# Kernel tuning notes

Hardware: AMD Instinct MI355X
Metric: run time of the kernel (lower is better)

The kernel has to match this reference:

```python
import jax, jax.numpy as jnp
import numpy as np

BN_EPS = 1e-5
SAMPLE_KEY = jax.random.key(42)


def setup_inputs() -> dict:
    key = jax.random.key(0)
    ks = jax.random.split(key, 12)
    B, W, E = 524288, 8, 4
    D = W * E  # 32, input dim of fc1

    def lin(k, fan_in, fan_out):
        k1, k2 = jax.random.split(k)
        bound = 1.0 / np.sqrt(fan_in)
        w = jax.random.uniform(k1, (fan_in, fan_out), jnp.float32, -bound, bound)
        b = jax.random.uniform(k2, (fan_out,), jnp.float32, -bound, bound)
        return w, b

    W1, b1 = lin(ks[0], D, 50)
    W2, b2 = lin(ks[1], 50, 30)
    W3, b3 = lin(ks[2], 30, 20)
    W4, b4 = lin(ks[3], 20, 15)
    W5, b5 = lin(ks[4], 15, W)
    # BatchNorm affine params (eval mode, running_mean=0, running_var=1)
    g1, be1 = jnp.ones((50,), jnp.float32), jnp.zeros((50,), jnp.float32)
    g2, be2 = jnp.ones((30,), jnp.float32), jnp.zeros((30,), jnp.float32)
    g3, be3 = jnp.ones((20,), jnp.float32), jnp.zeros((20,), jnp.float32)
    events = jax.random.normal(ks[5], (B, W, E), jnp.float32)
    return {"events": events,
            "W1": W1, "b1": b1, "g1": g1, "be1": be1,
            "W2": W2, "b2": b2, "g2": g2, "be2": be2,
            "W3": W3, "b3": b3, "g3": g3, "be3": be3,
            "W4": W4, "b4": b4, "W5": W5, "b5": b5}


def _bn_eval(x, g, b):
    # eval-mode BatchNorm1d with running_mean=0, running_var=1
    return x * (g / jnp.sqrt(1.0 + BN_EPS)) + b


def _probs(events, W1, b1, g1, be1, W2, b2, g2, be2, W3, b3, g3, be3, W4, b4, W5, b5):
    B = events.shape[0]
    x = events.reshape(B, -1)  # (B, window*event_size)
    h = jax.nn.relu(_bn_eval(x @ W1 + b1, g1, be1))
    h = jax.nn.relu(_bn_eval(h @ W2 + b2, g2, be2))
    h = jax.nn.relu(_bn_eval(h @ W3 + b3, g3, be3))
    h = jax.nn.relu(h @ W4 + b4)
    return jax.nn.sigmoid(h @ W5 + b5)  # (B, window_size)


def reference(events, W1, b1, g1, be1, W2, b2, g2, be2, W3, b3, g3, be3, W4, b4, W5, b5):
    p = _probs(events, W1, b1, g1, be1, W2, b2, g2, be2, W3, b3, g3, be3, W4, b4, W5, b5)
    # np.random.choice([0,1], p=[p, 1-p]) => P(choice=1) = 1 - p
    choice = jax.random.bernoulli(SAMPLE_KEY, 1.0 - p).astype(p.dtype)  # (B, W)
    chosen_events_np = 1.0 - choice
    flipped = jnp.abs(choice - p)            # prob of sampled outcome per element
    log_prob = jnp.log(jnp.prod(flipped, axis=1))  # (B,)
    return chosen_events_np, log_prob
```

## Files before the change

### kernel.cpp

```cpp
#include <hip/hip_runtime.h>
#include <math.h>

#define THREADS 256
#define P_MARGIN 1e-4f
#define FIXCAP 32

typedef float v2f __attribute__((ext_vector_type(2)));

__device__ __forceinline__ void tf2x32(unsigned x0, unsigned x1,
                                       unsigned &o0, unsigned &o1) {
  const unsigned k0 = 0u;
  const unsigned k1 = 42u;
  const unsigned k2 = 0x1BD11BDAu ^ k0 ^ k1;
  x0 += k0; x1 += k1;
#define TF_R(r) { x0 += x1; x1 = (x1 << (r)) | (x1 >> (32 - (r))); x1 ^= x0; }
  TF_R(13) TF_R(15) TF_R(26) TF_R(6)
  x0 += k1; x1 += k2 + 1u;
  TF_R(17) TF_R(29) TF_R(16) TF_R(24)
  x0 += k2; x1 += k0 + 2u;
  TF_R(13) TF_R(15) TF_R(26) TF_R(6)
  x0 += k0; x1 += k1 + 3u;
  TF_R(17) TF_R(29) TF_R(16) TF_R(24)
  x0 += k1; x1 += k2 + 4u;
  TF_R(13) TF_R(15) TF_R(26) TF_R(6)
  x0 += k2; x1 += k0 + 5u;
#undef TF_R
  o0 = x0; o1 = x1;
}

__global__ __launch_bounds__(THREADS, 4)
void wtf_kernel(const float* __restrict__ events,
                const float* __restrict__ W1, const float* __restrict__ b1,
                const float* __restrict__ g1, const float* __restrict__ be1,
                const float* __restrict__ W2, const float* __restrict__ b2,
                const float* __restrict__ g2, const float* __restrict__ be2,
                const float* __restrict__ W3, const float* __restrict__ b3,
                const float* __restrict__ g3, const float* __restrict__ be3,
                const float* __restrict__ W4, const float* __restrict__ b4,
                const float* __restrict__ W5, const float* __restrict__ b5,
                float* __restrict__ out_chosen,
                float* __restrict__ out_logp,
                int B) {
  __shared__ unsigned s_cnt;
  __shared__ unsigned s_rows[FIXCAP];
  __shared__ double sA[64];
  __shared__ double sB[64];
  __shared__ double sF[8];

  const int t = threadIdx.x;
  if (t == 0) s_cnt = 0;
  __syncthreads();

  const int b = blockIdx.x * THREADS + t;
  const bool active = (b < B);
  const float rden = (float)(1.0 / sqrt(1.0 + 1e-5));

  if (active) {
    float x[32];
    const float4* ev4 = reinterpret_cast<const float4*>(events) + (size_t)b * 8;
#pragma unroll
    for (int q = 0; q < 8; ++q) {
      float4 v = ev4[q];
      x[4 * q + 0] = v.x; x[4 * q + 1] = v.y; x[4 * q + 2] = v.z; x[4 * q + 3] = v.w;
    }

    v2f A[25];
#pragma unroll
    for (int j = 0; j < 25; ++j) A[j] = v2f{b1[2 * j], b1[2 * j + 1]};
#pragma unroll
    for (int k = 0; k < 32; ++k) {
      const v2f xk2 = {x[k], x[k]};
#pragma unroll
      for (int j = 0; j < 25; ++j) {
        v2f w = {W1[k * 50 + 2 * j], W1[k * 50 + 2 * j + 1]};
        A[j] = __builtin_elementwise_fma(xk2, w, A[j]);
      }
    }
    float a1[50];
#pragma unroll
    for (int j = 0; j < 25; ++j) {
      a1[2 * j + 0] = fmaxf(fmaf(A[j].x, g1[2 * j + 0] * rden, be1[2 * j + 0]), 0.f);
      a1[2 * j + 1] = fmaxf(fmaf(A[j].y, g1[2 * j + 1] * rden, be1[2 * j + 1]), 0.f);
    }

    v2f C[15];
#pragma unroll
    for (int j = 0; j < 15; ++j) C[j] = v2f{b2[2 * j], b2[2 * j + 1]};
#pragma unroll
    for (int k = 0; k < 50; ++k) {
      const v2f hk2 = {a1[k], a1[k]};
#pragma unroll
      for (int j = 0; j < 15; ++j) {
        v2f w = {W2[k * 30 + 2 * j], W2[k * 30 + 2 * j + 1]};
        C[j] = __builtin_elementwise_fma(hk2, w, C[j]);
      }
    }
    float a2[30];
#pragma unroll
    for (int j = 0; j < 15; ++j) {
      a2[2 * j + 0] = fmaxf(fmaf(C[j].x, g2[2 * j + 0] * rden, be2[2 * j + 0]), 0.f);
      a2[2 * j + 1] = fmaxf(fmaf(C[j].y, g2[2 * j + 1] * rden, be2[2 * j + 1]), 0.f);
    }

    v2f D[10];
#pragma unroll
    for (int j = 0; j < 10; ++j) D[j] = v2f{b3[2 * j], b3[2 * j + 1]};
#pragma unroll
    for (int k = 0; k < 30; ++k) {
      const v2f hk2 = {a2[k], a2[k]};
#pragma unroll
      for (int j = 0; j < 10; ++j) {
        v2f w = {W3[k * 20 + 2 * j], W3[k * 20 + 2 * j + 1]};
        D[j] = __builtin_elementwise_fma(hk2, w, D[j]);
      }
    }
    float a3[20];
#pragma unroll
    for (int j = 0; j < 10; ++j) {
      a3[2 * j + 0] = fmaxf(fmaf(D[j].x, g3[2 * j + 0] * rden, be3[2 * j + 0]), 0.f);
      a3[2 * j + 1] = fmaxf(fmaf(D[j].y, g3[2 * j + 1] * rden, be3[2 * j + 1]), 0.f);
    }

    v2f E[7];
    float e14 = b4[14];
#pragma unroll
    for (int j = 0; j < 7; ++j) E[j] = v2f{b4[2 * j], b4[2 * j + 1]};
#pragma unroll
    for (int k = 0; k < 20; ++k) {
      const float hk = a3[k];
      const v2f hk2 = {hk, hk};
#pragma unroll
      for (int j = 0; j < 7; ++j) {
        v2f w = {W4[k * 15 + 2 * j], W4[k * 15 + 2 * j + 1]};
        E[j] = __builtin_elementwise_fma(hk2, w, E[j]);
      }
      e14 = fmaf(hk, W4[k * 15 + 14], e14);
    }
    float a4[15];
#pragma unroll
    for (int j = 0; j < 7; ++j) {
      a4[2 * j + 0] = fmaxf(E[j].x, 0.f);
      a4[2 * j + 1] = fmaxf(E[j].y, 0.f);
    }
    a4[14] = fmaxf(e14, 0.f);

    v2f P[4];
#pragma unroll
    for (int j = 0; j < 4; ++j) P[j] = v2f{b5[2 * j], b5[2 * j + 1]};
#pragma unroll
    for (int k = 0; k < 15; ++k) {
      const v2f hk2 = {a4[k], a4[k]};
#pragma unroll
      for (int j = 0; j < 4; ++j) {
        v2f w = {W5[k * 8 + 2 * j], W5[k * 8 + 2 * j + 1]};
        P[j] = __builtin_elementwise_fma(hk2, w, P[j]);
      }
    }
    float p[8];
#pragma unroll
    for (int j = 0; j < 4; ++j) {
      p[2 * j + 0] = 1.f / (1.f + expf(-P[j].x));
      p[2 * j + 1] = 1.f / (1.f + expf(-P[j].y));
    }

    bool need = false;
    float prod = 1.f;
    float ch[8];
#pragma unroll
    for (int w = 0; w < 8; ++w) {
      unsigned j = 8u * (unsigned)b + (unsigned)w, o0, o1;
      tf2x32(0u, j, o0, o1);
      unsigned bits = o0 ^ o1;
      float u = __uint_as_float(0x3F800000u | (bits >> 9)) - 1.f;
      float thr = 1.f - p[w];
      bool choice = u < thr;
      need = need || (fabsf(u - thr) < P_MARGIN);
      ch[w] = choice ? 0.f : 1.f;
      prod *= choice ? thr : p[w];
    }
    if (need) {
      unsigned i = atomicAdd(&s_cnt, 1u);
      if (i < FIXCAP) s_rows[i] = (unsigned)b;
    }

    float4* oc = reinterpret_cast<float4*>(out_chosen) + (size_t)b * 2;
    oc[0] = make_float4(ch[0], ch[1], ch[2], ch[3]);
    oc[1] = make_float4(ch[4], ch[5], ch[6], ch[7]);
    out_logp[b] = logf(prod);
  }

  __syncthreads();
  unsigned cnt = s_cnt;
  if (cnt > FIXCAP) cnt = FIXCAP;
  if (cnt == 0) return;

  const double denom = sqrt(1.0 + 1e-5);
  for (unsigned r = 0; r < cnt; ++r) {
    const int rb = (int)s_rows[r];

    if (t < 32) sA[t] = (double)events[(size_t)rb * 32 + t];
    __syncthreads();

    double v = 0.0;
    if (t < 50) {
#pragma unroll
      for (int k = 0; k < 32; ++k) v = fma(sA[k], (double)W1[k * 50 + t], v);
      v += (double)b1[t];
      v = v * ((double)g1[t] / denom) + (double)be1[t];
      v = v > 0.0 ? v : 0.0;
    }
    __syncthreads();
    if (t < 50) sB[t] = v;
    __syncthreads();

    v = 0.0;
    if (t < 30) {
#pragma unroll
      for (int k = 0; k < 50; ++k) v = fma(sB[k], (double)W2[k * 30 + t], v);
      v += (double)b2[t];
      v = v * ((double)g2[t] / denom) + (double)be2[t];
      v = v > 0.0 ? v : 0.0;
    }
    __syncthreads();
    if (t < 30) sA[t] = v;
    __syncthreads();

    v = 0.0;
    if (t < 20) {
#pragma unroll
      for (int k = 0; k < 30; ++k) v = fma(sA[k], (double)W3[k * 20 + t], v);
      v += (double)b3[t];
      v = v * ((double)g3[t] / denom) + (double)be3[t];
      v = v > 0.0 ? v : 0.0;
    }
    __syncthreads();
    if (t < 20) sB[t] = v;
    __syncthreads();

    v = 0.0;
    if (t < 15) {
#pragma unroll
      for (int k = 0; k < 20; ++k) v = fma(sB[k], (double)W4[k * 15 + t], v);
      v += (double)b4[t];
      v = v > 0.0 ? v : 0.0;
    }
    __syncthreads();
    if (t < 15) sA[t] = v;
    __syncthreads();

    if (t < 8) {
      v = 0.0;
#pragma unroll
      for (int k = 0; k < 15; ++k) v = fma(sA[k], (double)W5[k * 8 + t], v);
      v += (double)b5[t];
      double p = 1.0 / (1.0 + exp(-v));
      unsigned j = 8u * (unsigned)rb + (unsigned)t, o0, o1;
      tf2x32(0u, j, o0, o1);
      unsigned bits = o0 ^ o1;
      float u = __uint_as_float(0x3F800000u | (bits >> 9)) - 1.f;
      double thr = 1.0 - p;
      bool choice = ((double)u < thr);
      out_chosen[(size_t)rb * 8 + t] = choice ? 0.f : 1.f;
      sF[t] = choice ? thr : p;
    }
    __syncthreads();
    if (t == 0) {
      double prod = 1.0;
      for (int w = 0; w < 8; ++w) prod *= sF[w];
      out_logp[rb] = (float)log(prod);
    }
    __syncthreads();
  }
}

extern "C" void kernel_launch(void* const* d_in, const int* in_sizes, int n_in,
                              void* d_out, int out_size, void* d_ws, size_t ws_size,
                              hipStream_t stream) {
  const float* events = (const float*)d_in[0];
  const float* W1  = (const float*)d_in[1];
  const float* b1  = (const float*)d_in[2];
  const float* g1  = (const float*)d_in[3];
  const float* be1 = (const float*)d_in[4];
  const float* W2  = (const float*)d_in[5];
  const float* b2  = (const float*)d_in[6];
  const float* g2  = (const float*)d_in[7];
  const float* be2 = (const float*)d_in[8];
  const float* W3  = (const float*)d_in[9];
  const float* b3  = (const float*)d_in[10];
  const float* g3  = (const float*)d_in[11];
  const float* be3 = (const float*)d_in[12];
  const float* W4  = (const float*)d_in[13];
  const float* b4  = (const float*)d_in[14];
  const float* W5  = (const float*)d_in[15];
  const float* b5  = (const float*)d_in[16];

  const int B = in_sizes[0] / 32;
  float* out = (float*)d_out;
  float* out_chosen = out;
  float* out_logp   = out + (size_t)B * 8;

  const int blocks = (B + THREADS - 1) / THREADS;
  hipLaunchKernelGGL(wtf_kernel, dim3(blocks), dim3(THREADS), 0, stream,
                     events, W1, b1, g1, be1, W2, b2, g2, be2,
                     W3, b3, g3, be3, W4, b4, W5, b5,
                     out_chosen, out_logp, B);
}
```

Baseline: 234.2 us.

## Split borderline-sample fixup into a separate kernel using a global worklist

The fused kernel is split in two. The fast kernel computes the fp32 MLP and sampling, then appends borderline rows to a global worklist in workspace through a global atomic. A second small kernel recomputes only those rows in double precision, spread across 512 blocks. This removes the shared-memory bookkeeping and block-wide barriers from the hot kernel and stops one block from serializing its own fixups, at the cost of an extra memset and kernel launch.

Measured after the change: 236.5 us. No clear change (+1.0%).

```diff
diff --git a/kernel.cpp b/kernel.cpp
--- a/kernel.cpp
+++ b/kernel.cpp
@@ -3,7 +3,6 @@
 
 #define THREADS 256
 #define P_MARGIN 1e-4f
-#define FIXCAP 32
 
 typedef float v2f __attribute__((ext_vector_type(2)));
 
@@ -29,176 +28,188 @@
 }
 
 __global__ __launch_bounds__(THREADS, 4)
-void wtf_kernel(const float* __restrict__ events,
-                const float* __restrict__ W1, const float* __restrict__ b1,
-                const float* __restrict__ g1, const float* __restrict__ be1,
-                const float* __restrict__ W2, const float* __restrict__ b2,
-                const float* __restrict__ g2, const float* __restrict__ be2,
-                const float* __restrict__ W3, const float* __restrict__ b3,
-                const float* __restrict__ g3, const float* __restrict__ be3,
-                const float* __restrict__ W4, const float* __restrict__ b4,
-                const float* __restrict__ W5, const float* __restrict__ b5,
-                float* __restrict__ out_chosen,
-                float* __restrict__ out_logp,
-                int B) {
-  __shared__ unsigned s_cnt;
-  __shared__ unsigned s_rows[FIXCAP];
+void wtf_fast_kernel(const float* __restrict__ events,
+                     const float* __restrict__ W1, const float* __restrict__ b1,
+                     const float* __restrict__ g1, const float* __restrict__ be1,
+                     const float* __restrict__ W2, const float* __restrict__ b2,
+                     const float* __restrict__ g2, const float* __restrict__ be2,
+                     const float* __restrict__ W3, const float* __restrict__ b3,
+                     const float* __restrict__ g3, const float* __restrict__ be3,
+                     const float* __restrict__ W4, const float* __restrict__ b4,
+                     const float* __restrict__ W5, const float* __restrict__ b5,
+                     float* __restrict__ out_chosen,
+                     float* __restrict__ out_logp,
+                     unsigned* __restrict__ fixlist,
+                     unsigned fixcap,
+                     int B) {
+  const int b = blockIdx.x * THREADS + threadIdx.x;
+  if (b >= B) return;
+
+  const float rden = (float)(1.0 / sqrt(1.0 + 1e-5));
+
+  float x[32];
+  const float4* ev4 = reinterpret_cast<const float4*>(events) + (size_t)b * 8;
+#pragma unroll
+  for (int q = 0; q < 8; ++q) {
+    float4 v = ev4[q];
+    x[4 * q + 0] = v.x; x[4 * q + 1] = v.y; x[4 * q + 2] = v.z; x[4 * q + 3] = v.w;
+  }
+
+  v2f A[25];
+#pragma unroll
+  for (int j = 0; j < 25; ++j) A[j] = v2f{b1[2 * j], b1[2 * j + 1]};
+#pragma unroll
+  for (int k = 0; k < 32; ++k) {
+    const v2f xk2 = {x[k], x[k]};
+#pragma unroll
+    for (int j = 0; j < 25; ++j) {
+      v2f w = {W1[k * 50 + 2 * j], W1[k * 50 + 2 * j + 1]};
+      A[j] = __builtin_elementwise_fma(xk2, w, A[j]);
+    }
+  }
+  float a1[50];
+#pragma unroll
+  for (int j = 0; j < 25; ++j) {
+    a1[2 * j + 0] = fmaxf(fmaf(A[j].x, g1[2 * j + 0] * rden, be1[2 * j + 0]), 0.f);
+    a1[2 * j + 1] = fmaxf(fmaf(A[j].y, g1[2 * j + 1] * rden, be1[2 * j + 1]), 0.f);
+  }
+
+  v2f C[15];
+#pragma unroll
+  for (int j = 0; j < 15; ++j) C[j] = v2f{b2[2 * j], b2[2 * j + 1]};
+#pragma unroll
+  for (int k = 0; k < 50; ++k) {
+    const v2f hk2 = {a1[k], a1[k]};
+#pragma unroll
+    for (int j = 0; j < 15; ++j) {
+      v2f w = {W2[k * 30 + 2 * j], W2[k * 30 + 2 * j + 1]};
+      C[j] = __builtin_elementwise_fma(hk2, w, C[j]);
+    }
+  }
+  float a2[30];
+#pragma unroll
+  for (int j = 0; j < 15; ++j) {
+    a2[2 * j + 0] = fmaxf(fmaf(C[j].x, g2[2 * j + 0] * rden, be2[2 * j + 0]), 0.f);
+    a2[2 * j + 1] = fmaxf(fmaf(C[j].y, g2[2 * j + 1] * rden, be2[2 * j + 1]), 0.f);
+  }
+
+  v2f D[10];
+#pragma unroll
+  for (int j = 0; j < 10; ++j) D[j] = v2f{b3[2 * j], b3[2 * j + 1]};
+#pragma unroll
+  for (int k = 0; k < 30; ++k) {
+    const v2f hk2 = {a2[k], a2[k]};
+#pragma unroll
+    for (int j = 0; j < 10; ++j) {
+      v2f w = {W3[k * 20 + 2 * j], W3[k * 20 + 2 * j + 1]};
+      D[j] = __builtin_elementwise_fma(hk2, w, D[j]);
+    }
+  }
+  float a3[20];
+#pragma unroll
+  for (int j = 0; j < 10; ++j) {
+    a3[2 * j + 0] = fmaxf(fmaf(D[j].x, g3[2 * j + 0] * rden, be3[2 * j + 0]), 0.f);
+    a3[2 * j + 1] = fmaxf(fmaf(D[j].y, g3[2 * j + 1] * rden, be3[2 * j + 1]), 0.f);
+  }
+
+  v2f E[7];
+  float e14 = b4[14];
+#pragma unroll
+  for (int j = 0; j < 7; ++j) E[j] = v2f{b4[2 * j], b4[2 * j + 1]};
+#pragma unroll
+  for (int k = 0; k < 20; ++k) {
+    const float hk = a3[k];
+    const v2f hk2 = {hk, hk};
+#pragma unroll
+    for (int j = 0; j < 7; ++j) {
+      v2f w = {W4[k * 15 + 2 * j], W4[k * 15 + 2 * j + 1]};
+      E[j] = __builtin_elementwise_fma(hk2, w, E[j]);
+    }
+    e14 = fmaf(hk, W4[k * 15 + 14], e14);
+  }
+  float a4[15];
+#pragma unroll
+  for (int j = 0; j < 7; ++j) {
+    a4[2 * j + 0] = fmaxf(E[j].x, 0.f);
+    a4[2 * j + 1] = fmaxf(E[j].y, 0.f);
+  }
+  a4[14] = fmaxf(e14, 0.f);
+
+  v2f P[4];
+#pragma unroll
+  for (int j = 0; j < 4; ++j) P[j] = v2f{b5[2 * j], b5[2 * j + 1]};
+#pragma unroll
+  for (int k = 0; k < 15; ++k) {
+    const v2f hk2 = {a4[k], a4[k]};
+#pragma unroll
+    for (int j = 0; j < 4; ++j) {
+      v2f w = {W5[k * 8 + 2 * j], W5[k * 8 + 2 * j + 1]};
+      P[j] = __builtin_elementwise_fma(hk2, w, P[j]);
+    }
+  }
+  float p[8];
+#pragma unroll
+  for (int j = 0; j < 4; ++j) {
+    p[2 * j + 0] = 1.f / (1.f + expf(-P[j].x));
+    p[2 * j + 1] = 1.f / (1.f + expf(-P[j].y));
+  }
+
+  bool need = false;
+  float prod = 1.f;
+  float ch[8];
+#pragma unroll
+  for (int w = 0; w < 8; ++w) {
+    unsigned j = 8u * (unsigned)b + (unsigned)w, o0, o1;
+    tf2x32(0u, j, o0, o1);
+    unsigned bits = o0 ^ o1;
+    float u = __uint_as_float(0x3F800000u | (bits >> 9)) - 1.f;
+    float thr = 1.f - p[w];
+    bool choice = u < thr;
+    need = need || (fabsf(u - thr) < P_MARGIN);
+    ch[w] = choice ? 0.f : 1.f;
+    prod *= choice ? thr : p[w];
+  }
+  if (need) {
+    unsigned i = atomicAdd(&fixlist[0], 1u);
+    if (i < fixcap) fixlist[1 + i] = (unsigned)b;
+  }
+
+  float4* oc = reinterpret_cast<float4*>(out_chosen) + (size_t)b * 2;
+  oc[0] = make_float4(ch[0], ch[1], ch[2], ch[3]);
+  oc[1] = make_float4(ch[4], ch[5], ch[6], ch[7]);
+  out_logp[b] = logf(prod);
+}
+
+__global__ __launch_bounds__(64, 4)
+void wtf_fix_kernel(const float* __restrict__ events,
+                    const float* __restrict__ W1, const float* __restrict__ b1,
+                    const float* __restrict__ g1, const float* __restrict__ be1,
+                    const float* __restrict__ W2, const float* __restrict__ b2,
+                    const float* __restrict__ g2, const float* __restrict__ be2,
+                    const float* __restrict__ W3, const float* __restrict__ b3,
+                    const float* __restrict__ g3, const float* __restrict__ be3,
+                    const float* __restrict__ W4, const float* __restrict__ b4,
+                    const float* __restrict__ W5, const float* __restrict__ b5,
+                    float* __restrict__ out_chosen,
+                    float* __restrict__ out_logp,
+                    const unsigned* __restrict__ fixlist,
+                    unsigned fixcap,
+                    int B) {
+  const unsigned raw = fixlist[0];
+  const unsigned cnt = raw < fixcap ? raw : fixcap;
+  if (blockIdx.x >= cnt) return;
+
   __shared__ double sA[64];
   __shared__ double sB[64];
   __shared__ double sF[8];
 
   const int t = threadIdx.x;
-  if (t == 0) s_cnt = 0;
-  __syncthreads();
-
-  const int b = blockIdx.x * THREADS + t;
-  const bool active = (b < B);
-  const float rden = (float)(1.0 / sqrt(1.0 + 1e-5));
-
-  if (active) {
-    float x[32];
-    const float4* ev4 = reinterpret_cast<const float4*>(events) + (size_t)b * 8;
-#pragma unroll
-    for (int q = 0; q < 8; ++q) {
-      float4 v = ev4[q];
-      x[4 * q + 0] = v.x; x[4 * q + 1] = v.y; x[4 * q + 2] = v.z; x[4 * q + 3] = v.w;
-    }
-
-    v2f A[25];
-#pragma unroll
-    for (int j = 0; j < 25; ++j) A[j] = v2f{b1[2 * j], b1[2 * j + 1]};
-#pragma unroll
-    for (int k = 0; k < 32; ++k) {
-      const v2f xk2 = {x[k], x[k]};
-#pragma unroll
-      for (int j = 0; j < 25; ++j) {
-        v2f w = {W1[k * 50 + 2 * j], W1[k * 50 + 2 * j + 1]};
-        A[j] = __builtin_elementwise_fma(xk2, w, A[j]);
-      }
-    }
-    float a1[50];
-#pragma unroll
-    for (int j = 0; j < 25; ++j) {
-      a1[2 * j + 0] = fmaxf(fmaf(A[j].x, g1[2 * j + 0] * rden, be1[2 * j + 0]), 0.f);
-      a1[2 * j + 1] = fmaxf(fmaf(A[j].y, g1[2 * j + 1] * rden, be1[2 * j + 1]), 0.f);
-    }
-
-    v2f C[15];
-#pragma unroll
-    for (int j = 0; j < 15; ++j) C[j] = v2f{b2[2 * j], b2[2 * j + 1]};
-#pragma unroll
-    for (int k = 0; k < 50; ++k) {
-      const v2f hk2 = {a1[k], a1[k]};
-#pragma unroll
-      for (int j = 0; j < 15; ++j) {
-        v2f w = {W2[k * 30 + 2 * j], W2[k * 30 + 2 * j + 1]};
-        C[j] = __builtin_elementwise_fma(hk2, w, C[j]);
-      }
-    }
-    float a2[30];
-#pragma unroll
-    for (int j = 0; j < 15; ++j) {
-      a2[2 * j + 0] = fmaxf(fmaf(C[j].x, g2[2 * j + 0] * rden, be2[2 * j + 0]), 0.f);
-      a2[2 * j + 1] = fmaxf(fmaf(C[j].y, g2[2 * j + 1] * rden, be2[2 * j + 1]), 0.f);
-    }
-
-    v2f D[10];
-#pragma unroll
-    for (int j = 0; j < 10; ++j) D[j] = v2f{b3[2 * j], b3[2 * j + 1]};
-#pragma unroll
-    for (int k = 0; k < 30; ++k) {
-      const v2f hk2 = {a2[k], a2[k]};
-#pragma unroll
-      for (int j = 0; j < 10; ++j) {
-        v2f w = {W3[k * 20 + 2 * j], W3[k * 20 + 2 * j + 1]};
-        D[j] = __builtin_elementwise_fma(hk2, w, D[j]);
-      }
-    }
-    float a3[20];
-#pragma unroll
-    for (int j = 0; j < 10; ++j) {
-      a3[2 * j + 0] = fmaxf(fmaf(D[j].x, g3[2 * j + 0] * rden, be3[2 * j + 0]), 0.f);
-      a3[2 * j + 1] = fmaxf(fmaf(D[j].y, g3[2 * j + 1] * rden, be3[2 * j + 1]), 0.f);
-    }
-
-    v2f E[7];
-    float e14 = b4[14];
-#pragma unroll
-    for (int j = 0; j < 7; ++j) E[j] = v2f{b4[2 * j], b4[2 * j + 1]};
-#pragma unroll
-    for (int k = 0; k < 20; ++k) {
-      const float hk = a3[k];
-      const v2f hk2 = {hk, hk};
-#pragma unroll
-      for (int j = 0; j < 7; ++j) {
-        v2f w = {W4[k * 15 + 2 * j], W4[k * 15 + 2 * j + 1]};
-        E[j] = __builtin_elementwise_fma(hk2, w, E[j]);
-      }
-      e14 = fmaf(hk, W4[k * 15 + 14], e14);
-    }
-    float a4[15];
-#pragma unroll
-    for (int j = 0; j < 7; ++j) {
-      a4[2 * j + 0] = fmaxf(E[j].x, 0.f);
-      a4[2 * j + 1] = fmaxf(E[j].y, 0.f);
-    }
-    a4[14] = fmaxf(e14, 0.f);
-
-    v2f P[4];
-#pragma unroll
-    for (int j = 0; j < 4; ++j) P[j] = v2f{b5[2 * j], b5[2 * j + 1]};
-#pragma unroll
-    for (int k = 0; k < 15; ++k) {
-      const v2f hk2 = {a4[k], a4[k]};
-#pragma unroll
-      for (int j = 0; j < 4; ++j) {
-        v2f w = {W5[k * 8 + 2 * j], W5[k * 8 + 2 * j + 1]};
-        P[j] = __builtin_elementwise_fma(hk2, w, P[j]);
-      }
-    }
-    float p[8];
-#pragma unroll
-    for (int j = 0; j < 4; ++j) {
-      p[2 * j + 0] = 1.f / (1.f + expf(-P[j].x));
-      p[2 * j + 1] = 1.f / (1.f + expf(-P[j].y));
-    }
-
-    bool need = false;
-    float prod = 1.f;
-    float ch[8];
-#pragma unroll
-    for (int w = 0; w < 8; ++w) {
-      unsigned j = 8u * (unsigned)b + (unsigned)w, o0, o1;
-      tf2x32(0u, j, o0, o1);
-      unsigned bits = o0 ^ o1;
-      float u = __uint_as_float(0x3F800000u | (bits >> 9)) - 1.f;
-      float thr = 1.f - p[w];
-      bool choice = u < thr;
-      need = need || (fabsf(u - thr) < P_MARGIN);
-      ch[w] = choice ? 0.f : 1.f;
-      prod *= choice ? thr : p[w];
-    }
-    if (need) {
-      unsigned i = atomicAdd(&s_cnt, 1u);
-      if (i < FIXCAP) s_rows[i] = (unsigned)b;
-    }
-
-    float4* oc = reinterpret_cast<float4*>(out_chosen) + (size_t)b * 2;
-    oc[0] = make_float4(ch[0], ch[1], ch[2], ch[3]);
-    oc[1] = make_float4(ch[4], ch[5], ch[6], ch[7]);
-    out_logp[b] = logf(prod);
-  }
-
-  __syncthreads();
-  unsigned cnt = s_cnt;
-  if (cnt > FIXCAP) cnt = FIXCAP;
-  if (cnt == 0) return;
-
   const double denom = sqrt(1.0 + 1e-5);
-  for (unsigned r = 0; r < cnt; ++r) {
-    const int rb = (int)s_rows[r];
-
-    if (t < 32) sA[t] = (double)events[(size_t)rb * 32 + t];
+
+  for (unsigned idx = blockIdx.x; idx < cnt; idx += gridDim.x) {
+    const int b = (int)fixlist[1 + idx];
+
+    if (t < 32) sA[t] = (double)events[(size_t)b * 32 + t];
     __syncthreads();
 
     double v = 0.0;
@@ -254,20 +265,20 @@
       for (int k = 0; k < 15; ++k) v = fma(sA[k], (double)W5[k * 8 + t], v);
       v += (double)b5[t];
       double p = 1.0 / (1.0 + exp(-v));
-      unsigned j = 8u * (unsigned)rb + (unsigned)t, o0, o1;
+      unsigned j = 8u * (unsigned)b + (unsigned)t, o0, o1;
       tf2x32(0u, j, o0, o1);
       unsigned bits = o0 ^ o1;
       float u = __uint_as_float(0x3F800000u | (bits >> 9)) - 1.f;
       double thr = 1.0 - p;
       bool choice = ((double)u < thr);
-      out_chosen[(size_t)rb * 8 + t] = choice ? 0.f : 1.f;
+      out_chosen[(size_t)b * 8 + t] = choice ? 0.f : 1.f;
       sF[t] = choice ? thr : p;
     }
     __syncthreads();
     if (t == 0) {
       double prod = 1.0;
       for (int w = 0; w < 8; ++w) prod *= sF[w];
-      out_logp[rb] = (float)log(prod);
+      out_logp[b] = (float)log(prod);
     }
     __syncthreads();
   }
@@ -298,10 +309,19 @@
   float* out = (float*)d_out;
   float* out_chosen = out;
   float* out_logp   = out + (size_t)B * 8;
+  unsigned* fixlist = (unsigned*)d_ws;
+  unsigned fixcap = (unsigned)(ws_size / sizeof(unsigned) - 1);
+  if (fixcap > (unsigned)B) fixcap = (unsigned)B;
+
+  hipMemsetAsync(d_ws, 0, sizeof(unsigned), stream);
 
   const int blocks = (B + THREADS - 1) / THREADS;
-  hipLaunchKernelGGL(wtf_kernel, dim3(blocks), dim3(THREADS), 0, stream,
+  hipLaunchKernelGGL(wtf_fast_kernel, dim3(blocks), dim3(THREADS), 0, stream,
                      events, W1, b1, g1, be1, W2, b2, g2, be2,
                      W3, b3, g3, be3, W4, b4, W5, b5,
-                     out_chosen, out_logp, B);
+                     out_chosen, out_logp, fixlist, fixcap, B);
+  hipLaunchKernelGGL(wtf_fix_kernel, dim3(512), dim3(64), 0, stream,
+                     events, W1, b1, g1, be1, W2, b2, g2, be2,
+                     W3, b3, g3, be3, W4, b4, W5, b5,
+                     out_chosen, out_logp, fixlist, fixcap, B);
 }
```
